# Kernel tuning notes

Measured on AMD Instinct MI355X. Metric: run time of the kernel, lower is better.

The kernel has to match this reference:

```python
import jax, jax.numpy as jnp
import numpy as np

NUM_BUCKETS = 32
MAX_DISTANCE = 128


def _relative_position_bucket(relative_position):
    # bidirectional=True variant of T5's bucketing
    n = -relative_position
    num_buckets = NUM_BUCKETS // 2
    ret = (n < 0).astype(jnp.int32) * num_buckets
    n = jnp.abs(n)
    max_exact = num_buckets // 2
    is_small = n < max_exact
    # log-spaced buckets for large distances
    val_if_large = max_exact + (
        jnp.log(jnp.maximum(n, 1).astype(jnp.float32) / max_exact)
        / np.log(MAX_DISTANCE / max_exact)
        * (num_buckets - max_exact)
    ).astype(jnp.int32)
    val_if_large = jnp.minimum(val_if_large, num_buckets - 1)
    return ret + jnp.where(is_small, n, val_if_large)


def setup_inputs() -> dict:
    key = jax.random.key(0)
    ks = jax.random.split(key, 6)
    B, S, D, H, DK = 4, 1024, 1024, 16, 64
    inner = H * DK
    s = 1.0 / np.sqrt(D).astype(np.float32)
    x = jax.random.normal(ks[0], (B, S, D), jnp.float32)
    Wq = jax.random.normal(ks[1], (D, inner), jnp.float32) * s
    Wk = jax.random.normal(ks[2], (D, inner), jnp.float32) * s
    Wv = jax.random.normal(ks[3], (D, inner), jnp.float32) * s
    Wo = jax.random.normal(ks[4], (inner, D), jnp.float32) * s
    rel_emb = jax.random.normal(ks[5], (NUM_BUCKETS, H), jnp.float32) * 0.02
    return {"x": x, "Wq": Wq, "Wk": Wk, "Wv": Wv, "Wo": Wo, "rel_emb": rel_emb}


def reference(x, Wq, Wk, Wv, Wo, rel_emb):
    B, S, D = x.shape
    H = rel_emb.shape[1]
    DK = Wq.shape[1] // H

    def shape_heads(t):  # [B,S,H*DK] -> [B,H,S,DK]
        return t.reshape(B, S, H, DK).transpose(0, 2, 1, 3)

    q = shape_heads(x @ Wq)
    k = shape_heads(x @ Wk)
    v = shape_heads(x @ Wv)

    # note: T5 does NOT scale by 1/sqrt(d_kv)
    scores = jnp.einsum("bhqd,bhkd->bhqk", q, k)

    pos = jnp.arange(S)
    rel = pos[None, :] - pos[:, None]            # memory - query
    bucket = _relative_position_bucket(rel)      # [S,S] int32
    bias = rel_emb[bucket].transpose(2, 0, 1)[None]  # [1,H,S,S]

    weights = jax.nn.softmax(scores + bias, axis=-1)
    ctx = jnp.einsum("bhqk,bhkd->bhqd", weights, v)
    ctx = ctx.transpose(0, 2, 1, 3).reshape(B, S, H * DK)
    return ctx @ Wo
```

## Files before the change

kernel.cpp:

```cpp
#include <hip/hip_runtime.h>
#include <math.h>

#define B_ 4
#define S_ 1024
#define D_ 1024
#define H_ 16
#define DK_ 64

typedef short bf16x8 __attribute__((ext_vector_type(8)));
typedef float f32x4 __attribute__((ext_vector_type(4)));

__device__ __forceinline__ unsigned short f2bf(float f) {
    unsigned int u = __float_as_uint(f);
    u = (u + 0x7FFFu + ((u >> 16) & 1u)) >> 16;
    return (unsigned short)u;
}

__device__ __forceinline__ float exp2_fast(float x) {
#if __has_builtin(__builtin_amdgcn_exp2f)
    return __builtin_amdgcn_exp2f(x);
#else
    return exp2f(x);
#endif
}

__device__ __forceinline__ unsigned pack_bf16(float a, float b) {
#if __has_builtin(__builtin_amdgcn_cvt_pk_bf16_f32)
    auto v = __builtin_amdgcn_cvt_pk_bf16_f32(a, b);
    return __builtin_bit_cast(unsigned int, v);
#else
    return (unsigned)f2bf(a) | ((unsigned)f2bf(b) << 16);
#endif
}

__device__ __forceinline__ void gl2lds16(const void* g, void* l) {
    typedef unsigned int u32;
    auto gp = (const __attribute__((address_space(1))) u32*)(unsigned long long)g;
    auto lp = (__attribute__((address_space(3))) u32*)(unsigned int)(unsigned long long)l;
    __builtin_amdgcn_global_load_lds(gp, lp, 16, 0, 0);
}

#define LOG2E 1.44269504f
#define BIAS_OFF 20.0f

__global__ __launch_bounds__(256) void conv_x(const float* __restrict__ x,
                                              unsigned short* __restrict__ xb) {
    int i = (blockIdx.x * 256 + threadIdx.x) * 4;
    float4 v = *(const float4*)&x[i];
    ushort4 o;
    o.x = f2bf(v.x); o.y = f2bf(v.y); o.z = f2bf(v.z); o.w = f2bf(v.w);
    *(ushort4*)&xb[i] = o;
}

__global__ __launch_bounds__(256) void conv_wt(
    const float* __restrict__ W0, const float* __restrict__ W1,
    const float* __restrict__ W2, const float* __restrict__ W3,
    unsigned short* __restrict__ Wts)
{
    const float* W = (blockIdx.y == 0) ? W0 : (blockIdx.y == 1) ? W1
                   : (blockIdx.y == 2) ? W2 : W3;
    unsigned short* Wt = Wts + (size_t)blockIdx.y * 1048576;

    __shared__ float T[32][33];
    const int t = threadIdx.x;
    const int tile = blockIdx.x;
    const int k0 = (tile >> 5) * 32, n0 = (tile & 31) * 32;
    {
        int r = t >> 3, c4 = (t & 7) * 4;
        float4 v = *(const float4*)&W[(size_t)(k0 + r) * D_ + n0 + c4];
        T[r][c4 + 0] = v.x; T[r][c4 + 1] = v.y; T[r][c4 + 2] = v.z; T[r][c4 + 3] = v.w;
    }
    __syncthreads();
    {
        int rn = t >> 3, c4 = (t & 7) * 4;
        ushort4 o;
        o.x = f2bf(T[c4 + 0][rn]); o.y = f2bf(T[c4 + 1][rn]);
        o.z = f2bf(T[c4 + 2][rn]); o.w = f2bf(T[c4 + 3][rn]);
        *(ushort4*)&Wt[(size_t)(n0 + rn) * D_ + k0 + c4] = o;
    }
}

__global__ __launch_bounds__(256) void gemm_qkv(
    const unsigned short* __restrict__ xb,
    const unsigned short* __restrict__ Wts,
    unsigned short* __restrict__ Qb, unsigned short* __restrict__ Kb,
    unsigned short* __restrict__ Vtb)
{
    const int z = blockIdx.z;
    const unsigned short* Bt = Wts + (size_t)z * 1048576;

    __shared__ __align__(16) unsigned short Ast[128][32];
    __shared__ __align__(16) unsigned short Bst[128][32];

    const int tid = threadIdx.x;
    const int wave = tid >> 6, lane = tid & 63;
    const int quad = lane >> 4, l16 = lane & 15;
    const int wm = (wave & 1) * 64, wn = (wave >> 1) * 64;
    const int row0 = blockIdx.y * 128, col0 = blockIdx.x * 128;
    const int lr = lane >> 2, lc = (lane & 3) * 8;

    f32x4 acc[4][4];
#pragma unroll
    for (int i = 0; i < 4; i++)
#pragma unroll
        for (int j = 0; j < 4; j++) acc[i][j] = 0;

    for (int k0 = 0; k0 < D_; k0 += 32) {
        __syncthreads();
#pragma unroll
        for (int c = 0; c < 2; c++) {
            int m = wave * 32 + c * 16;
            gl2lds16(&xb[(size_t)(row0 + m + lr) * D_ + k0 + lc], &Ast[m][0]);
            gl2lds16(&Bt[(size_t)(col0 + m + lr) * D_ + k0 + lc], &Bst[m][0]);
        }
        __syncthreads();

        bf16x8 af[4], bfr[4];
#pragma unroll
        for (int mt = 0; mt < 4; mt++)
            af[mt] = *(const bf16x8*)&Ast[wm + mt * 16 + l16][quad * 8];
#pragma unroll
        for (int nt = 0; nt < 4; nt++)
            bfr[nt] = *(const bf16x8*)&Bst[wn + nt * 16 + l16][quad * 8];
#pragma unroll
        for (int mt = 0; mt < 4; mt++)
#pragma unroll
            for (int nt = 0; nt < 4; nt++)
                acc[mt][nt] = __builtin_amdgcn_mfma_f32_16x16x32_bf16(
                    af[mt], bfr[nt], acc[mt][nt], 0, 0, 0);
    }

    const float scale = (z == 0) ? LOG2E : 1.0f;
#pragma unroll
    for (int mt = 0; mt < 4; mt++)
#pragma unroll
        for (int nt = 0; nt < 4; nt++)
#pragma unroll
            for (int reg = 0; reg < 4; reg++) {
                int row = row0 + wm + mt * 16 + quad * 4 + reg;
                int col = col0 + wn + nt * 16 + l16;
                int b = row >> 10, s = row & 1023;
                int h = col >> 6, dk = col & 63;
                unsigned short v = f2bf(acc[mt][nt][reg] * scale);
                if (z == 0)      Qb[(((size_t)(b * H_ + h)) * S_ + s) * DK_ + dk] = v;
                else if (z == 1) Kb[(((size_t)(b * H_ + h)) * S_ + s) * DK_ + dk] = v;
                else             Vtb[(((size_t)(b * H_ + h)) * DK_ + dk) * S_ + s] = v;
            }
}

__global__ __launch_bounds__(256) void gemm_out(
    const unsigned short* __restrict__ Ab,
    const unsigned short* __restrict__ Bt,
    float* __restrict__ out)
{
    __shared__ __align__(16) unsigned short Ast[128][32];
    __shared__ __align__(16) unsigned short Bst[128][32];

    const int tid = threadIdx.x;
    const int wave = tid >> 6, lane = tid & 63;
    const int quad = lane >> 4, l16 = lane & 15;
    const int wm = (wave & 1) * 64, wn = (wave >> 1) * 64;
    const int row0 = blockIdx.y * 128, col0 = blockIdx.x * 128;
    const int lr = lane >> 2, lc = (lane & 3) * 8;

    f32x4 acc[4][4];
#pragma unroll
    for (int i = 0; i < 4; i++)
#pragma unroll
        for (int j = 0; j < 4; j++) acc[i][j] = 0;

    for (int k0 = 0; k0 < D_; k0 += 32) {
        __syncthreads();
#pragma unroll
        for (int c = 0; c < 2; c++) {
            int m = wave * 32 + c * 16;
            gl2lds16(&Ab[(size_t)(row0 + m + lr) * D_ + k0 + lc], &Ast[m][0]);
            gl2lds16(&Bt[(size_t)(col0 + m + lr) * D_ + k0 + lc], &Bst[m][0]);
        }
        __syncthreads();

        bf16x8 af[4], bfr[4];
#pragma unroll
        for (int mt = 0; mt < 4; mt++)
            af[mt] = *(const bf16x8*)&Ast[wm + mt * 16 + l16][quad * 8];
#pragma unroll
        for (int nt = 0; nt < 4; nt++)
            bfr[nt] = *(const bf16x8*)&Bst[wn + nt * 16 + l16][quad * 8];
#pragma unroll
        for (int mt = 0; mt < 4; mt++)
#pragma unroll
            for (int nt = 0; nt < 4; nt++)
                acc[mt][nt] = __builtin_amdgcn_mfma_f32_16x16x32_bf16(
                    af[mt], bfr[nt], acc[mt][nt], 0, 0, 0);
    }

#pragma unroll
    for (int mt = 0; mt < 4; mt++)
#pragma unroll
        for (int nt = 0; nt < 4; nt++)
#pragma unroll
            for (int reg = 0; reg < 4; reg++) {
                int row = row0 + wm + mt * 16 + quad * 4 + reg;
                int col = col0 + wn + nt * 16 + l16;
                out[(size_t)row * D_ + col] = acc[mt][nt][reg];
            }
}

__global__ __launch_bounds__(256) void attn_mfma(
    const unsigned short* __restrict__ Qb, const unsigned short* __restrict__ Kb,
    const unsigned short* __restrict__ Vtb, const float* __restrict__ rel_emb,
    unsigned short* __restrict__ CTXb)
{
    __shared__ __align__(16) unsigned short Ks[2][128][32];
    __shared__ __align__(16) unsigned short Vts[4][64][32];
    __shared__ __align__(16) unsigned short Pw[4][4][16][34];
    __shared__ float bias_tab[2047];

    const int b = blockIdx.z, h = blockIdx.y;
    const int q0 = blockIdx.x * 128;
    const int tid = threadIdx.x;
    const int wave = tid >> 6, lane = tid & 63;
    const int quad = lane >> 4, l16 = lane & 15;
    const int qw = q0 + wave * 32;

    for (int idx = tid; idx < 2047; idx += 256) {
        int rel = idx - 1023;
        int n = -rel, ret = 0;
        if (n < 0) { ret = 16; n = -n; }
        int bkt;
        if (n < 8) bkt = ret + n;
        else {
            float t = logf((float)n / 8.0f) / logf(16.0f) * 8.0f;
            int v = 8 + (int)t;
            if (v > 15) v = 15;
            bkt = ret + v;
        }
        bias_tab[idx] = rel_emb[bkt * H_ + h] * LOG2E - BIAS_OFF;
    }

    const size_t hb = (size_t)(b * H_ + h) * (S_ * DK_);
    const unsigned short* Qp = Qb + hb;
    const unsigned short* Kp = Kb + hb;
    const unsigned short* Vp = Vtb + hb;

    bf16x8 qf[2][2];
#pragma unroll
    for (int sub = 0; sub < 2; sub++)
#pragma unroll
        for (int ks = 0; ks < 2; ks++)
            qf[sub][ks] = *(const bf16x8*)
                &Qp[(size_t)(qw + sub * 16 + l16) * DK_ + ks * 32 + quad * 8];

    f32x4 O[2][4];
#pragma unroll
    for (int sub = 0; sub < 2; sub++)
#pragma unroll
        for (int dt = 0; dt < 4; dt++) O[sub][dt] = 0;
    float lsum[2][4] = {{0.f, 0.f, 0.f, 0.f}, {0.f, 0.f, 0.f, 0.f}};

    const int lr = lane >> 2, lc8 = (lane & 3) * 8;

    for (int kt = 0; kt < 8; kt++) {
        const int k0 = kt * 128;
        __syncthreads();
#pragma unroll
        for (int i = 0; i < 4; i++) {
            int idx = wave * 4 + i;
            {
                int s = idx >> 3, rg = idx & 7;
                gl2lds16(&Kp[(size_t)(k0 + rg * 16 + lr) * DK_ + s * 32 + lc8],
                         &Ks[s][rg * 16][0]);
            }
            {
                int qt = idx >> 2, rg = idx & 3;
                gl2lds16(&Vp[(size_t)(rg * 16 + lr) * S_ + k0 + qt * 32 + lc8],
                         &Vts[qt][rg * 16][0]);
            }
        }
        __syncthreads();

#pragma unroll
        for (int sub = 0; sub < 2; sub++) {
            const int sb = qw + sub * 16;
            f32x4 sacc[8];
#pragma unroll
            for (int nt = 0; nt < 8; nt++) {
                f32x4 c;
#pragma unroll
                for (int reg = 0; reg < 4; reg++)
                    c[reg] = bias_tab[k0 + nt * 16 + l16 - (sb + quad * 4 + reg) + 1023];
                sacc[nt] = c;
            }
#pragma unroll
            for (int ks = 0; ks < 2; ks++)
#pragma unroll
                for (int nt = 0; nt < 8; nt++) {
                    bf16x8 kf = *(const bf16x8*)&Ks[ks][nt * 16 + l16][quad * 8];
                    sacc[nt] = __builtin_amdgcn_mfma_f32_16x16x32_bf16(
                        qf[sub][ks], kf, sacc[nt], 0, 0, 0);
                }

#pragma unroll
            for (int reg = 0; reg < 4; reg++) {
                const int r = quad * 4 + reg;
#pragma unroll
                for (int nt2 = 0; nt2 < 4; nt2++) {
                    float pa = exp2_fast(sacc[2 * nt2][reg]);
                    float pb = exp2_fast(sacc[2 * nt2 + 1][reg]);
                    lsum[sub][reg] += pa + pb;
                    unsigned u = pack_bf16(pa, pb);
                    Pw[wave][nt2][r][l16]      = (unsigned short)u;
                    Pw[wave][nt2][r][16 + l16] = (unsigned short)(u >> 16);
                }
            }

#pragma unroll
            for (int ks2 = 0; ks2 < 4; ks2++) {
                bf16x8 pf = *(const bf16x8*)&Pw[wave][ks2][l16][quad * 8];
#pragma unroll
                for (int dt = 0; dt < 4; dt++) {
                    bf16x8 vf = *(const bf16x8*)&Vts[ks2][dt * 16 + l16][quad * 8];
                    O[sub][dt] = __builtin_amdgcn_mfma_f32_16x16x32_bf16(
                        pf, vf, O[sub][dt], 0, 0, 0);
                }
            }
        }
    }

#pragma unroll
    for (int sub = 0; sub < 2; sub++)
#pragma unroll
        for (int reg = 0; reg < 4; reg++) {
            float l = lsum[sub][reg];
#pragma unroll
            for (int off = 1; off < 16; off <<= 1)
                l += __shfl_xor(l, off);
            float inv = 1.0f / l;
            int s = qw + sub * 16 + quad * 4 + reg;
#pragma unroll
            for (int dt = 0; dt < 4; dt++) {
                int col = h * DK_ + dt * 16 + l16;
                CTXb[((size_t)(b * S_ + s)) * D_ + col] = f2bf(O[sub][dt][reg] * inv);
            }
        }
}

extern "C" void kernel_launch(void* const* d_in, const int* in_sizes, int n_in,
                              void* d_out, int out_size, void* d_ws, size_t ws_size,
                              hipStream_t stream) {
    const float* x   = (const float*)d_in[0];
    const float* Wq  = (const float*)d_in[1];
    const float* Wk  = (const float*)d_in[2];
    const float* Wv  = (const float*)d_in[3];
    const float* Wo  = (const float*)d_in[4];
    const float* rel = (const float*)d_in[5];
    float* out = (float*)d_out;

    unsigned short* ws = (unsigned short*)d_ws;
    unsigned short* xb   = ws;
    unsigned short* Wts  = ws + (size_t)4194304;
    unsigned short* Qb   = ws + (size_t)8388608;
    unsigned short* Kb   = ws + (size_t)12582912;
    unsigned short* Vtb  = ws + (size_t)16777216;
    unsigned short* CTXb = ws + (size_t)20971520;

    conv_x<<<4096, 256, 0, stream>>>(x, xb);
    conv_wt<<<dim3(1024, 4), 256, 0, stream>>>(Wq, Wk, Wv, Wo, Wts);
    gemm_qkv<<<dim3(8, 32, 3), 256, 0, stream>>>(xb, Wts, Qb, Kb, Vtb);
    attn_mfma<<<dim3(8, 16, 4), 256, 0, stream>>>(Qb, Kb, Vtb, rel, CTXb);
    gemm_out<<<dim3(8, 32), 256, 0, stream>>>(CTXb, Wts + (size_t)3 * 1048576, out);
}
```

Before: 196.7 us.

## Deepen GEMM K-step and restructure attention loop with packed DPP P-writes

Both projection GEMMs now stage 64 K-elements per barrier pair instead of 32, halving the number of syncs per tile. The attention inner loop is reordered to iterate over 32-key chunks outermost, so K and V fragments are loaded once and reused across both query sub-tiles. The P tile shrinks to a single per-wave 16x40 buffer written as packed 32-bit words, using a DPP lane-xor swap to pair neighbouring values. Bias reads are restructured into four contiguous loads. This risks extra LDS reuse hazards in the shared per-wave P buffer and more register pressure from held fragments.

```diff
diff --git a/kernel.cpp b/kernel.cpp
--- a/kernel.cpp
+++ b/kernel.cpp
@@ -30,6 +30,16 @@
     return __builtin_bit_cast(unsigned int, v);
 #else
     return (unsigned)f2bf(a) | ((unsigned)f2bf(b) << 16);
+#endif
+}
+
+__device__ __forceinline__ float dpp_xor1(float x) {
+#if __has_builtin(__builtin_amdgcn_update_dpp)
+    int i = __builtin_bit_cast(int, x);
+    int r = __builtin_amdgcn_update_dpp(0, i, 0xB1, 0xF, 0xF, true);
+    return __builtin_bit_cast(float, r);
+#else
+    return __shfl_xor(x, 1);
 #endif
 }
 
@@ -89,8 +99,8 @@
     const int z = blockIdx.z;
     const unsigned short* Bt = Wts + (size_t)z * 1048576;
 
-    __shared__ __align__(16) unsigned short Ast[128][32];
-    __shared__ __align__(16) unsigned short Bst[128][32];
+    __shared__ __align__(16) unsigned short Ast[2][128][32];
+    __shared__ __align__(16) unsigned short Bst[2][128][32];
 
     const int tid = threadIdx.x;
     const int wave = tid >> 6, lane = tid & 63;
@@ -105,29 +115,35 @@
 #pragma unroll
         for (int j = 0; j < 4; j++) acc[i][j] = 0;
 
-    for (int k0 = 0; k0 < D_; k0 += 32) {
-        __syncthreads();
-#pragma unroll
-        for (int c = 0; c < 2; c++) {
-            int m = wave * 32 + c * 16;
-            gl2lds16(&xb[(size_t)(row0 + m + lr) * D_ + k0 + lc], &Ast[m][0]);
-            gl2lds16(&Bt[(size_t)(col0 + m + lr) * D_ + k0 + lc], &Bst[m][0]);
-        }
-        __syncthreads();
-
-        bf16x8 af[4], bfr[4];
-#pragma unroll
-        for (int mt = 0; mt < 4; mt++)
-            af[mt] = *(const bf16x8*)&Ast[wm + mt * 16 + l16][quad * 8];
-#pragma unroll
-        for (int nt = 0; nt < 4; nt++)
-            bfr[nt] = *(const bf16x8*)&Bst[wn + nt * 16 + l16][quad * 8];
-#pragma unroll
-        for (int mt = 0; mt < 4; mt++)
+    for (int k0 = 0; k0 < D_; k0 += 64) {
+        __syncthreads();
+#pragma unroll
+        for (int i = 0; i < 4; i++) {
+            int idx = wave * 4 + i;
+            int ks = idx >> 3, rg = idx & 7;
+            gl2lds16(&xb[(size_t)(row0 + rg * 16 + lr) * D_ + k0 + ks * 32 + lc],
+                     &Ast[ks][rg * 16][0]);
+            gl2lds16(&Bt[(size_t)(col0 + rg * 16 + lr) * D_ + k0 + ks * 32 + lc],
+                     &Bst[ks][rg * 16][0]);
+        }
+        __syncthreads();
+
+#pragma unroll
+        for (int ks = 0; ks < 2; ks++) {
+            bf16x8 af[4], bfr[4];
+#pragma unroll
+            for (int mt = 0; mt < 4; mt++)
+                af[mt] = *(const bf16x8*)&Ast[ks][wm + mt * 16 + l16][quad * 8];
 #pragma unroll
             for (int nt = 0; nt < 4; nt++)
-                acc[mt][nt] = __builtin_amdgcn_mfma_f32_16x16x32_bf16(
-                    af[mt], bfr[nt], acc[mt][nt], 0, 0, 0);
+                bfr[nt] = *(const bf16x8*)&Bst[ks][wn + nt * 16 + l16][quad * 8];
+#pragma unroll
+            for (int mt = 0; mt < 4; mt++)
+#pragma unroll
+                for (int nt = 0; nt < 4; nt++)
+                    acc[mt][nt] = __builtin_amdgcn_mfma_f32_16x16x32_bf16(
+                        af[mt], bfr[nt], acc[mt][nt], 0, 0, 0);
+        }
     }
 
     const float scale = (z == 0) ? LOG2E : 1.0f;
@@ -153,8 +169,8 @@
     const unsigned short* __restrict__ Bt,
     float* __restrict__ out)
 {
-    __shared__ __align__(16) unsigned short Ast[128][32];
-    __shared__ __align__(16) unsigned short Bst[128][32];
+    __shared__ __align__(16) unsigned short Ast[2][128][32];
+    __shared__ __align__(16) unsigned short Bst[2][128][32];
 
     const int tid = threadIdx.x;
     const int wave = tid >> 6, lane = tid & 63;
@@ -169,29 +185,35 @@
 #pragma unroll
         for (int j = 0; j < 4; j++) acc[i][j] = 0;
 
-    for (int k0 = 0; k0 < D_; k0 += 32) {
-        __syncthreads();
-#pragma unroll
-        for (int c = 0; c < 2; c++) {
-            int m = wave * 32 + c * 16;
-            gl2lds16(&Ab[(size_t)(row0 + m + lr) * D_ + k0 + lc], &Ast[m][0]);
-            gl2lds16(&Bt[(size_t)(col0 + m + lr) * D_ + k0 + lc], &Bst[m][0]);
-        }
-        __syncthreads();
-
-        bf16x8 af[4], bfr[4];
-#pragma unroll
-        for (int mt = 0; mt < 4; mt++)
-            af[mt] = *(const bf16x8*)&Ast[wm + mt * 16 + l16][quad * 8];
-#pragma unroll
-        for (int nt = 0; nt < 4; nt++)
-            bfr[nt] = *(const bf16x8*)&Bst[wn + nt * 16 + l16][quad * 8];
-#pragma unroll
-        for (int mt = 0; mt < 4; mt++)
+    for (int k0 = 0; k0 < D_; k0 += 64) {
+        __syncthreads();
+#pragma unroll
+        for (int i = 0; i < 4; i++) {
+            int idx = wave * 4 + i;
+            int ks = idx >> 3, rg = idx & 7;
+            gl2lds16(&Ab[(size_t)(row0 + rg * 16 + lr) * D_ + k0 + ks * 32 + lc],
+                     &Ast[ks][rg * 16][0]);
+            gl2lds16(&Bt[(size_t)(col0 + rg * 16 + lr) * D_ + k0 + ks * 32 + lc],
+                     &Bst[ks][rg * 16][0]);
+        }
+        __syncthreads();
+
+#pragma unroll
+        for (int ks = 0; ks < 2; ks++) {
+            bf16x8 af[4], bfr[4];
+#pragma unroll
+            for (int mt = 0; mt < 4; mt++)
+                af[mt] = *(const bf16x8*)&Ast[ks][wm + mt * 16 + l16][quad * 8];
 #pragma unroll
             for (int nt = 0; nt < 4; nt++)
-                acc[mt][nt] = __builtin_amdgcn_mfma_f32_16x16x32_bf16(
-                    af[mt], bfr[nt], acc[mt][nt], 0, 0, 0);
+                bfr[nt] = *(const bf16x8*)&Bst[ks][wn + nt * 16 + l16][quad * 8];
+#pragma unroll
+            for (int mt = 0; mt < 4; mt++)
+#pragma unroll
+                for (int nt = 0; nt < 4; nt++)
+                    acc[mt][nt] = __builtin_amdgcn_mfma_f32_16x16x32_bf16(
+                        af[mt], bfr[nt], acc[mt][nt], 0, 0, 0);
+        }
     }
 
 #pragma unroll
@@ -213,7 +235,7 @@
 {
     __shared__ __align__(16) unsigned short Ks[2][128][32];
     __shared__ __align__(16) unsigned short Vts[4][64][32];
-    __shared__ __align__(16) unsigned short Pw[4][4][16][34];
+    __shared__ __align__(16) unsigned short Pw[4][16][40];
     __shared__ float bias_tab[2047];
 
     const int b = blockIdx.z, h = blockIdx.y;
@@ -259,6 +281,8 @@
     float lsum[2][4] = {{0.f, 0.f, 0.f, 0.f}, {0.f, 0.f, 0.f, 0.f}};
 
     const int lr = lane >> 2, lc8 = (lane & 3) * 8;
+    const int pcol = (l16 & 1) ? (8 + (l16 >> 1)) : (l16 >> 1);
+    unsigned* pwp = (unsigned*)&Pw[wave][0][0];
 
     for (int kt = 0; kt < 8; kt++) {
         const int k0 = kt * 128;
@@ -280,49 +304,54 @@
         __syncthreads();
 
 #pragma unroll
-        for (int sub = 0; sub < 2; sub++) {
-            const int sb = qw + sub * 16;
-            f32x4 sacc[8];
-#pragma unroll
-            for (int nt = 0; nt < 8; nt++) {
-                f32x4 c;
-#pragma unroll
-                for (int reg = 0; reg < 4; reg++)
-                    c[reg] = bias_tab[k0 + nt * 16 + l16 - (sb + quad * 4 + reg) + 1023];
-                sacc[nt] = c;
-            }
-#pragma unroll
-            for (int ks = 0; ks < 2; ks++)
-#pragma unroll
-                for (int nt = 0; nt < 8; nt++) {
-                    bf16x8 kf = *(const bf16x8*)&Ks[ks][nt * 16 + l16][quad * 8];
-                    sacc[nt] = __builtin_amdgcn_mfma_f32_16x16x32_bf16(
-                        qf[sub][ks], kf, sacc[nt], 0, 0, 0);
+        for (int nt2 = 0; nt2 < 4; nt2++) {
+            bf16x8 kf[2][2], vf[4];
+#pragma unroll
+            for (int t = 0; t < 2; t++)
+#pragma unroll
+                for (int ks = 0; ks < 2; ks++)
+                    kf[t][ks] = *(const bf16x8*)
+                        &Ks[ks][(2 * nt2 + t) * 16 + l16][quad * 8];
+#pragma unroll
+            for (int dt = 0; dt < 4; dt++)
+                vf[dt] = *(const bf16x8*)&Vts[nt2][dt * 16 + l16][quad * 8];
+
+#pragma unroll
+            for (int sub = 0; sub < 2; sub++) {
+                const int sb = qw + sub * 16;
+                f32x4 sacc[2];
+#pragma unroll
+                for (int t = 0; t < 2; t++) {
+                    int b0 = 1023 + k0 + (2 * nt2 + t) * 16 + l16 - (sb + quad * 4 + 3);
+                    float bl[4];
+#pragma unroll
+                    for (int j = 0; j < 4; j++) bl[j] = bias_tab[b0 + j];
+#pragma unroll
+                    for (int reg = 0; reg < 4; reg++) sacc[t][reg] = bl[3 - reg];
                 }
-
-#pragma unroll
-            for (int reg = 0; reg < 4; reg++) {
-                const int r = quad * 4 + reg;
-#pragma unroll
-                for (int nt2 = 0; nt2 < 4; nt2++) {
-                    float pa = exp2_fast(sacc[2 * nt2][reg]);
-                    float pb = exp2_fast(sacc[2 * nt2 + 1][reg]);
+#pragma unroll
+                for (int ks = 0; ks < 2; ks++)
+#pragma unroll
+                    for (int t = 0; t < 2; t++)
+                        sacc[t] = __builtin_amdgcn_mfma_f32_16x16x32_bf16(
+                            qf[sub][ks], kf[t][ks], sacc[t], 0, 0, 0);
+
+#pragma unroll
+                for (int reg = 0; reg < 4; reg++) {
+                    float pa = exp2_fast(sacc[0][reg]);
+                    float pb = exp2_fast(sacc[1][reg]);
                     lsum[sub][reg] += pa + pb;
-                    unsigned u = pack_bf16(pa, pb);
-                    Pw[wave][nt2][r][l16]      = (unsigned short)u;
-                    Pw[wave][nt2][r][16 + l16] = (unsigned short)(u >> 16);
+                    float pax = dpp_xor1(pa), pbx = dpp_xor1(pb);
+                    unsigned ue = pack_bf16(pa, pax);
+                    unsigned uo = pack_bf16(pbx, pb);
+                    pwp[(quad * 4 + reg) * 20 + pcol] = (l16 & 1) ? uo : ue;
                 }
-            }
-
-#pragma unroll
-            for (int ks2 = 0; ks2 < 4; ks2++) {
-                bf16x8 pf = *(const bf16x8*)&Pw[wave][ks2][l16][quad * 8];
-#pragma unroll
-                for (int dt = 0; dt < 4; dt++) {
-                    bf16x8 vf = *(const bf16x8*)&Vts[ks2][dt * 16 + l16][quad * 8];
+
+                bf16x8 pf = *(const bf16x8*)&Pw[wave][l16][quad * 8];
+#pragma unroll
+                for (int dt = 0; dt < 4; dt++)
                     O[sub][dt] = __builtin_amdgcn_mfma_f32_16x16x32_bf16(
-                        pf, vf, O[sub][dt], 0, 0, 0);
-                }
+                        pf, vf[dt], O[sub][dt], 0, 0, 0);
             }
         }
     }
```

Result: slower. 214.2 us (+8.9%).
